# Optimization experiments

Measured on AMD Instinct MI355X. Metric: run time of the kernel, lower is better.

Reference implementation:

```python
import jax, jax.numpy as jnp
import numpy as np

B, S, D = 2, 1024, 1024
H, HD = 16, 64          # n_heads, head_dim (H*HD == D)
E, FF = 8, 2816         # num_experts, moe hidden_dim
TOP_K = 2               # hard-coded torch.topk(scores, 2)
EPS = 1e-5


def rmsnorm(x, w):
    return x * jax.lax.rsqrt(jnp.mean(x * x, axis=-1, keepdims=True) + EPS) * w


def apply_rope(x, cos, sin):
    # x: [B,S,H,HD]; cos/sin: [S,HD//2] -> interleaved rotary (llama style)
    xr, xi = x[..., 0::2], x[..., 1::2]
    c = cos[None, :, None, :]
    s = sin[None, :, None, :]
    out_r = xr * c - xi * s
    out_i = xr * s + xi * c
    return jnp.stack([out_r, out_i], axis=-1).reshape(x.shape)


def setup_inputs() -> dict:
    key = jax.random.key(0)
    ks = jax.random.split(key, 10)
    sc = 0.02
    pos = jnp.arange(S, dtype=jnp.float32)
    inv = 1.0 / (10000.0 ** (jnp.arange(0, HD, 2, dtype=jnp.float32) / HD))
    ang = pos[:, None] * inv[None, :]                       # [S, HD//2]
    return {
        "x": jax.random.normal(ks[0], (B, S, D), jnp.float32),
        "freqs_cos": jnp.cos(ang),
        "freqs_sin": jnp.sin(ang),
        "attn_norm_w": jnp.ones((D,), jnp.float32),
        "wq": jax.random.normal(ks[1], (D, D), jnp.float32) * sc,
        "wk": jax.random.normal(ks[2], (D, D), jnp.float32) * sc,
        "wv": jax.random.normal(ks[3], (D, D), jnp.float32) * sc,
        "wo": jax.random.normal(ks[4], (D, D), jnp.float32) * sc,
        "ffn_norm_w": jnp.ones((D,), jnp.float32),
        "gate_w": jax.random.normal(ks[5], (E, D), jnp.float32) * sc,
        "w1": jax.random.normal(ks[6], (E, FF, D), jnp.float32) * sc,
        "w2": jax.random.normal(ks[7], (E, FF, D), jnp.float32) * sc,
        "w3": jax.random.normal(ks[8], (E, FF, D), jnp.float32) * sc,
    }


def reference(x, freqs_cos, freqs_sin, attn_norm_w, wq, wk, wv, wo,
              ffn_norm_w, gate_w, w1, w2, w3):
    b, s, d = x.shape

    # ---- pre-norm attention + residual ----
    xn = rmsnorm(x, attn_norm_w)
    q = (xn @ wq.T).reshape(b, s, H, HD)
    k = (xn @ wk.T).reshape(b, s, H, HD)
    v = (xn @ wv.T).reshape(b, s, H, HD)
    q = apply_rope(q, freqs_cos, freqs_sin)
    k = apply_rope(k, freqs_cos, freqs_sin)
    scores = jnp.einsum("bqhd,bkhd->bhqk", q, k) / jnp.sqrt(jnp.float32(HD))
    causal = jnp.tril(jnp.ones((s, s), bool))
    scores = jnp.where(causal[None, None], scores, jnp.finfo(scores.dtype).min)
    attn = jax.nn.softmax(scores, axis=-1)
    o = jnp.einsum("bhqk,bkhd->bqhd", attn, v).reshape(b, s, d) @ wo.T
    h = x + o

    # ---- top-2 MoE FFN (math identical to gather-per-token einsums) ----
    t = rmsnorm(h, ffn_norm_w).reshape(-1, d)               # [T, D]
    T = t.shape[0]
    gate = t @ gate_w.T                                     # [T, E]
    expert_weights, expert_idx = jax.lax.top_k(gate, TOP_K)
    expert_weights = jax.nn.softmax(expert_weights, axis=-1)  # [T, 2]

    x1 = jax.nn.silu(jnp.einsum("td,efd->tef", t, w1))      # [T, E, FF]
    x3 = jnp.einsum("td,efd->tef", t, w3)                   # [T, E, FF]
    ta = jnp.arange(T)[:, None]
    g = x1[ta, expert_idx] * x3[ta, expert_idx]             # [T, 2, FF]
    gw = g * expert_weights[..., None]                      # fold routing weights
    h_full = jnp.zeros((T, E, FF), t.dtype).at[ta, expert_idx].add(gw)
    moe = jnp.einsum("tef,efd->td", h_full, w2)             # [T, D]

    return h + moe.reshape(b, s, d)
```

## Files before the change

### kernel.cpp

```cpp
#include <hip/hip_runtime.h>

#define DI __device__ __forceinline__

typedef __attribute__((ext_vector_type(8))) short short8;
typedef __attribute__((ext_vector_type(4))) float f32x4;

#define DM   1024
#define TT   2048
#define SEQ  1024
#define NHD  16
#define HDD  64
#define NE   8
#define FF   2816

DI ushort f2bf(float f){
  union { float f; unsigned u; } c; c.f = f;
  unsigned u = c.u;
  u += 0x7fffu + ((u >> 16) & 1u);
  return (ushort)(u >> 16);
}
DI float bf2f(ushort b){
  union { unsigned u; float f; } c; c.u = ((unsigned)b) << 16;
  return c.f;
}
DI unsigned pk2(float a, float b){ return (unsigned)f2bf(a) | ((unsigned)f2bf(b) << 16); }
DI uint2 mku2(unsigned a, unsigned b){ uint2 r; r.x = a; r.y = b; return r; }

DI f32x4 MFMA(short8 a, short8 b, f32x4 c){
  return __builtin_amdgcn_mfma_f32_16x16x32_bf16(a, b, c, 0, 0, 0);
}

DI void gload16(const void* g, void* l){
  __builtin_amdgcn_global_load_lds(
      (const __attribute__((address_space(1))) unsigned*)g,
      (__attribute__((address_space(3))) unsigned*)l, 16, 0, 0);
}

#define LDSWZB(row, p) (((row) * 128) + ((((p) ^ ((row) & 7))) * 16))

__global__ __launch_bounds__(256) void k_rmsnorm(const float* __restrict__ x,
                                                 const float* __restrict__ w,
                                                 ushort* __restrict__ xh,
                                                 ushort* __restrict__ xl)
{
  int row = blockIdx.x, tid = threadIdx.x;
  float4 v = ((const float4*)(x + (size_t)row * DM))[tid];
  float ss = v.x*v.x + v.y*v.y + v.z*v.z + v.w*v.w;
#pragma unroll
  for (int m = 32; m >= 1; m >>= 1) ss += __shfl_xor(ss, m);
  __shared__ float sh[4];
  if ((tid & 63) == 0) sh[tid >> 6] = ss;
  __syncthreads();
  ss = sh[0] + sh[1] + sh[2] + sh[3];
  float rstd = 1.0f / sqrtf(ss * (1.0f / DM) + 1e-5f);
  float4 wv = ((const float4*)w)[tid];
  float o0 = v.x * rstd * wv.x, o1 = v.y * rstd * wv.y;
  float o2 = v.z * rstd * wv.z, o3 = v.w * rstd * wv.w;
  ushort h0 = f2bf(o0), h1 = f2bf(o1), h2 = f2bf(o2), h3 = f2bf(o3);
  ((uint2*)(xh + (size_t)row * DM))[tid] =
      mku2((unsigned)h0 | ((unsigned)h1 << 16), (unsigned)h2 | ((unsigned)h3 << 16));
  ((uint2*)(xl + (size_t)row * DM))[tid] =
      mku2(pk2(o0 - bf2f(h0), o1 - bf2f(h1)), pk2(o2 - bf2f(h2), o3 - bf2f(h3)));
}

__global__ __launch_bounds__(256) void k_wsplit(
    const float* __restrict__ wq, const float* __restrict__ wk,
    const float* __restrict__ wv, const float* __restrict__ wo,
    ushort* __restrict__ qh, ushort* __restrict__ ql,
    ushort* __restrict__ kh, ushort* __restrict__ kl,
    ushort* __restrict__ vh, ushort* __restrict__ vl,
    ushort* __restrict__ oh, ushort* __restrict__ ol)
{
  int y = blockIdx.y;
  const float* W = y == 0 ? wq : (y == 1 ? wk : (y == 2 ? wv : wo));
  ushort* H = y == 0 ? qh : (y == 1 ? kh : (y == 2 ? vh : oh));
  ushort* L = y == 0 ? ql : (y == 1 ? kl : (y == 2 ? vl : ol));
  int i = blockIdx.x * 256 + threadIdx.x;
  float4 v = ((const float4*)W)[i];
  ushort h0 = f2bf(v.x), h1 = f2bf(v.y), h2 = f2bf(v.z), h3 = f2bf(v.w);
  ((uint2*)H)[i] = mku2((unsigned)h0 | ((unsigned)h1 << 16),
                        (unsigned)h2 | ((unsigned)h3 << 16));
  ((uint2*)L)[i] = mku2(pk2(v.x - bf2f(h0), v.y - bf2f(h1)),
                        pk2(v.z - bf2f(h2), v.w - bf2f(h3)));
}

__global__ __launch_bounds__(256, 2) void k_gemm_qkv(
    const ushort* __restrict__ xh, const ushort* __restrict__ xl,
    const ushort* __restrict__ wqh, const ushort* __restrict__ wql,
    const ushort* __restrict__ wkh, const ushort* __restrict__ wkl,
    const ushort* __restrict__ wvh, const ushort* __restrict__ wvl,
    float* __restrict__ qf, float* __restrict__ kf,
    ushort* __restrict__ vh, ushort* __restrict__ vl)
{
  __shared__ __align__(16) char lds[65536];
  char* Ah = lds;          char* Al = lds + 16384;
  char* Bh = lds + 32768;  char* Bl = lds + 49152;
  int bn = blockIdx.x, bm = blockIdx.y;
  int which = bn >> 3, bnn = bn & 7;
  const ushort* WH = which == 0 ? wqh : (which == 1 ? wkh : wvh);
  const ushort* WL = which == 0 ? wql : (which == 1 ? wkl : wvl);
  int tid = threadIdx.x, lane = tid & 63, w = tid >> 6, wr = w >> 1, wc = w & 1;
  int r0 = lane >> 3, pp = lane & 7;
  size_t asrc[4], bsrc[4]; int cdst[4];
#pragma unroll
  for (int i = 0; i < 4; i++) {
    int c = w * 4 + i;
    int row = c * 8 + r0;
    asrc[i] = (size_t)(bm * 128 + row) * DM + (pp ^ r0) * 8;
    bsrc[i] = (size_t)(bnn * 128 + row) * DM + (pp ^ r0) * 8;
    cdst[i] = c * 1024;
  }
  f32x4 acc[4][4] = {};
  for (int kb = 0; kb < DM; kb += 64) {
    __syncthreads();
#pragma unroll
    for (int i = 0; i < 4; i++) {
      gload16(xh + asrc[i] + kb, Ah + cdst[i]);
      gload16(xl + asrc[i] + kb, Al + cdst[i]);
      gload16(WH + bsrc[i] + kb, Bh + cdst[i]);
      gload16(WL + bsrc[i] + kb, Bl + cdst[i]);
    }
    __syncthreads();
#pragma unroll
    for (int kk = 0; kk < 2; kk++) {
      int j = kk * 4 + (lane >> 4);
      short8 ar[4], al[4];
#pragma unroll
      for (int mi = 0; mi < 4; mi++) {
        int row = wr * 64 + mi * 16 + (lane & 15);
        ar[mi] = *(const short8*)(Ah + LDSWZB(row, j));
        al[mi] = *(const short8*)(Al + LDSWZB(row, j));
      }
#pragma unroll
      for (int ni = 0; ni < 4; ni++) {
        int n = wc * 64 + ni * 16 + (lane & 15);
        short8 b_h = *(const short8*)(Bh + LDSWZB(n, j));
        short8 b_l = *(const short8*)(Bl + LDSWZB(n, j));
#pragma unroll
        for (int mi = 0; mi < 4; mi++) {
          acc[mi][ni] = MFMA(ar[mi], b_h, acc[mi][ni]);
          acc[mi][ni] = MFMA(al[mi], b_h, acc[mi][ni]);
          acc[mi][ni] = MFMA(ar[mi], b_l, acc[mi][ni]);
        }
      }
    }
  }
#pragma unroll
  for (int mi = 0; mi < 4; mi++)
#pragma unroll
    for (int ni = 0; ni < 4; ni++)
#pragma unroll
      for (int r = 0; r < 4; r++) {
        int rg = bm*128 + wr*64 + mi*16 + (lane >> 4)*4 + r;
        int cg = bnn*128 + wc*64 + ni*16 + (lane & 15);
        float v = acc[mi][ni][r];
        if (which == 0)      qf[(size_t)rg * DM + cg] = v;
        else if (which == 1) kf[(size_t)rg * DM + cg] = v;
        else {
          int b = rg >> 10, s = rg & 1023, hh = cg >> 6, hd = cg & 63;
          size_t o = ((size_t)((b*NHD + hh)*HDD + hd)) * SEQ + s;
          ushort hv = f2bf(v);
          vh[o] = hv; vl[o] = f2bf(v - bf2f(hv));
        }
      }
}

__global__ __launch_bounds__(256) void k_rope(
    const float* __restrict__ qf, const float* __restrict__ kf,
    const float* __restrict__ fc, const float* __restrict__ fs,
    ushort* __restrict__ qh, ushort* __restrict__ ql,
    ushort* __restrict__ kh, ushort* __restrict__ kl)
{
  int t = blockIdx.x, tid = threadIdx.x;
  int b = t >> 10, s = t & 1023;
#pragma unroll
  for (int i = 0; i < 2; i++) {
    int p = tid + i*256;
    int hh = p >> 5, pi = p & 31;
    float c = fc[s*32 + pi], sn = fs[s*32 + pi];
    size_t o = ((size_t)(b*NHD + hh) * SEQ + s) * HDD + pi*2;
    {
      float2 v = *(const float2*)(qf + (size_t)t * DM + hh*HDD + pi*2);
      float r0 = v.x*c - v.y*sn, r1 = v.x*sn + v.y*c;
      ushort a0 = f2bf(r0), a1 = f2bf(r1);
      *(unsigned*)(qh + o) = (unsigned)a0 | ((unsigned)a1 << 16);
      *(unsigned*)(ql + o) = pk2(r0 - bf2f(a0), r1 - bf2f(a1));
    }
    {
      float2 v = *(const float2*)(kf + (size_t)t * DM + hh*HDD + pi*2);
      float r0 = v.x*c - v.y*sn, r1 = v.x*sn + v.y*c;
      ushort a0 = f2bf(r0), a1 = f2bf(r1);
      *(unsigned*)(kh + o) = (unsigned)a0 | ((unsigned)a1 << 16);
      *(unsigned*)(kl + o) = pk2(r0 - bf2f(a0), r1 - bf2f(a1));
    }
  }
}

__global__ __launch_bounds__(256) void k_attn(
    const ushort* __restrict__ qh_, const ushort* __restrict__ ql_,
    const ushort* __restrict__ kh_, const ushort* __restrict__ kl_,
    const ushort* __restrict__ vh_, const ushort* __restrict__ vl_,
    ushort* __restrict__ oh_, ushort* __restrict__ ol_)
{
  __shared__ __align__(16) ushort Kh[64*64], Kl[64*64], Vh[64*64], Vl[64*64];
  __shared__ __align__(16) ushort Ph[4*16*64], Pl[4*16*64];
  int qt = blockIdx.x, bh = blockIdx.y;
  int tid = threadIdx.x, lane = tid & 63, w = tid >> 6;
  short8 qfh[2], qfl[2];
  int qrow = qt*64 + w*16 + (lane & 15);
#pragma unroll
  for (int ks = 0; ks < 2; ks++) {
    size_t g = ((size_t)bh * SEQ + qrow) * HDD + ks*32 + (lane >> 4)*8;
    qfh[ks] = *(const short8*)(qh_ + g);
    qfl[ks] = *(const short8*)(ql_ + g);
  }
  f32x4 oacc[4] = {};
  float mrun[4], lrun[4];
#pragma unroll
  for (int r = 0; r < 4; r++) { mrun[r] = -1e30f; lrun[r] = 0.0f; }

  for (int kt = 0; kt <= qt; kt++) {
    __syncthreads();
#pragma unroll
    for (int i = 0; i < 2; i++) {
      int c = tid + i*256, row = c >> 3, sl = c & 7;
      int d = row*64 + ((sl + row) & 7) * 8;
      size_t gk = ((size_t)bh * SEQ + kt*64 + row) * HDD + sl*8;
      *(uint4*)&Kh[d] = *(const uint4*)(kh_ + gk);
      *(uint4*)&Kl[d] = *(const uint4*)(kl_ + gk);
      size_t gv = ((size_t)bh * HDD + row) * SEQ + kt*64 + sl*8;
      *(uint4*)&Vh[d] = *(const uint4*)(vh_ + gv);
      *(uint4*)&Vl[d] = *(const uint4*)(vl_ + gv);
    }
    __syncthreads();
    f32x4 sa[4] = {};
#pragma unroll
    for (int j = 0; j < 4; j++) {
#pragma unroll
      for (int ks = 0; ks < 2; ks++) {
        int kr = j*16 + (lane & 15);
        int d = kr*64 + (((ks*4 + (lane >> 4)) + kr) & 7) * 8;
        short8 b_h = *(const short8*)&Kh[d];
        short8 b_l = *(const short8*)&Kl[d];
        sa[j] = MFMA(qfh[ks], b_h, sa[j]);
        sa[j] = MFMA(qfl[ks], b_h, sa[j]);
        sa[j] = MFMA(qfh[ks], b_l, sa[j]);
      }
    }
    float sv[4][4];
#pragma unroll
    for (int j = 0; j < 4; j++)
#pragma unroll
      for (int r = 0; r < 4; r++) {
        float xx = sa[j][r] * 0.125f;
        if (kt == qt) {
          int kv = j*16 + (lane & 15), qi = w*16 + (lane >> 4)*4 + r;
          if (kv > qi) xx = -1e30f;
        }
        sv[j][r] = xx;
      }
#pragma unroll
    for (int r = 0; r < 4; r++) {
      float mx = fmaxf(fmaxf(sv[0][r], sv[1][r]), fmaxf(sv[2][r], sv[3][r]));
#pragma unroll
      for (int m = 8; m >= 1; m >>= 1) mx = fmaxf(mx, __shfl_xor(mx, m));
      float mn = fmaxf(mrun[r], mx);
      float alp = __expf(mrun[r] - mn);
      mrun[r] = mn;
      float rs = 0.0f;
#pragma unroll
      for (int j = 0; j < 4; j++) { float pv = __expf(sv[j][r] - mn); sv[j][r] = pv; rs += pv; }
#pragma unroll
      for (int m = 8; m >= 1; m >>= 1) rs += __shfl_xor(rs, m);
      lrun[r] = lrun[r] * alp + rs;
#pragma unroll
      for (int hf = 0; hf < 4; hf++) oacc[hf][r] *= alp;
    }
#pragma unroll
    for (int j = 0; j < 4; j++)
#pragma unroll
      for (int r = 0; r < 4; r++) {
        int row = (lane >> 4)*4 + r, col = j*16 + (lane & 15);
        int d = w*1024 + row*64 + (((col >> 3) ^ (row & 7)) * 8) + (col & 7);
        ushort hv = f2bf(sv[j][r]);
        Ph[d] = hv; Pl[d] = f2bf(sv[j][r] - bf2f(hv));
      }
#pragma unroll
    for (int hf = 0; hf < 4; hf++) {
#pragma unroll
      for (int ks = 0; ks < 2; ks++) {
        int prow = lane & 15;
        int pg = ((ks*4 + (lane >> 4)) ^ (prow & 7)) * 8;
        short8 pfh = *(const short8*)&Ph[w*1024 + prow*64 + pg];
        short8 pfl = *(const short8*)&Pl[w*1024 + prow*64 + pg];
        int vrow = hf*16 + (lane & 15);
        int vd = vrow*64 + (((ks*4 + (lane >> 4)) + vrow) & 7) * 8;
        short8 vfh = *(const short8*)&Vh[vd];
        short8 vfl = *(const short8*)&Vl[vd];
        oacc[hf] = MFMA(pfh, vfh, oacc[hf]);
        oacc[hf] = MFMA(pfl, vfh, oacc[hf]);
        oacc[hf] = MFMA(pfh, vfl, oacc[hf]);
      }
    }
  }
  int b = bh >> 4, h = bh & 15;
#pragma unroll
  for (int r = 0; r < 4; r++) {
    float li = 1.0f / lrun[r];
    int srow = qt*64 + w*16 + (lane >> 4)*4 + r;
#pragma unroll
    for (int hf = 0; hf < 4; hf++) {
      float v = oacc[hf][r] * li;
      size_t o = ((size_t)(b*SEQ + srow)) * DM + h*HDD + hf*16 + (lane & 15);
      ushort hv = f2bf(v);
      oh_[o] = hv; ol_[o] = f2bf(v - bf2f(hv));
    }
  }
}

__global__ __launch_bounds__(256, 2) void k_gemm_wo(
    const ushort* __restrict__ oh, const ushort* __restrict__ ol,
    const ushort* __restrict__ woh, const ushort* __restrict__ wol,
    const float* __restrict__ x, float* __restrict__ hb)
{
  __shared__ __align__(16) char lds[49152];
  char* Ah = lds;          char* Al = lds + 8192;
  char* Bh = lds + 16384;  char* Bl = lds + 32768;
  int bnn = blockIdx.x, bm = blockIdx.y;
  int tid = threadIdx.x, lane = tid & 63, w = tid >> 6;
  int r0 = lane >> 3, pp = lane & 7;
  size_t asrc[2]; int adst[2];
#pragma unroll
  for (int i = 0; i < 2; i++) {
    int c = w * 2 + i;
    int row = c * 8 + r0;
    asrc[i] = (size_t)(bm * 64 + row) * DM + (pp ^ r0) * 8;
    adst[i] = c * 1024;
  }
  size_t bsrc[4]; int bdst[4];
#pragma unroll
  for (int i = 0; i < 4; i++) {
    int c = w * 4 + i;
    int row = c * 8 + r0;
    bsrc[i] = (size_t)(bnn * 128 + row) * DM + (pp ^ r0) * 8;
    bdst[i] = c * 1024;
  }
  f32x4 acc[4][2] = {};
  for (int kb = 0; kb < DM; kb += 64) {
    __syncthreads();
#pragma unroll
    for (int i = 0; i < 2; i++) {
      gload16(oh + asrc[i] + kb, Ah + adst[i]);
      gload16(ol + asrc[i] + kb, Al + adst[i]);
    }
#pragma unroll
    for (int i = 0; i < 4; i++) {
      gload16(woh + bsrc[i] + kb, Bh + bdst[i]);
      gload16(wol + bsrc[i] + kb, Bl + bdst[i]);
    }
    __syncthreads();
#pragma unroll
    for (int kk = 0; kk < 2; kk++) {
      int j = kk * 4 + (lane >> 4);
      short8 ar[4], al[4];
#pragma unroll
      for (int mi = 0; mi < 4; mi++) {
        int row = mi * 16 + (lane & 15);
        ar[mi] = *(const short8*)(Ah + LDSWZB(row, j));
        al[mi] = *(const short8*)(Al + LDSWZB(row, j));
      }
#pragma unroll
      for (int ni = 0; ni < 2; ni++) {
        int n = w * 32 + ni * 16 + (lane & 15);
        short8 b_h = *(const short8*)(Bh + LDSWZB(n, j));
        short8 b_l = *(const short8*)(Bl + LDSWZB(n, j));
#pragma unroll
        for (int mi = 0; mi < 4; mi++) {
          acc[mi][ni] = MFMA(ar[mi], b_h, acc[mi][ni]);
          acc[mi][ni] = MFMA(al[mi], b_h, acc[mi][ni]);
          acc[mi][ni] = MFMA(ar[mi], b_l, acc[mi][ni]);
        }
      }
    }
  }
#pragma unroll
  for (int mi = 0; mi < 4; mi++)
#pragma unroll
    for (int ni = 0; ni < 2; ni++)
#pragma unroll
      for (int r = 0; r < 4; r++) {
        int rg = bm*64 + mi*16 + (lane >> 4)*4 + r;
        int cg = bnn*128 + w*32 + ni*16 + (lane & 15);
        hb[(size_t)rg * DM + cg] = x[(size_t)rg * DM + cg] + acc[mi][ni][r];
      }
}

__global__ __launch_bounds__(256) void k_gate(
    const float* __restrict__ hb, const float* __restrict__ fw, const float* __restrict__ gwt,
    ushort* __restrict__ tb, int* __restrict__ idx, float* __restrict__ ew, int* __restrict__ cnt)
{
  int t = blockIdx.x, tid = threadIdx.x;
  float4 v = ((const float4*)(hb + (size_t)t * DM))[tid];
  float ss = v.x*v.x + v.y*v.y + v.z*v.z + v.w*v.w;
#pragma unroll
  for (int m = 32; m >= 1; m >>= 1) ss += __shfl_xor(ss, m);
  __shared__ float sh[4];
  if ((tid & 63) == 0) sh[tid >> 6] = ss;
  __syncthreads();
  ss = sh[0] + sh[1] + sh[2] + sh[3];
  float rstd = 1.0f / sqrtf(ss * (1.0f / DM) + 1e-5f);
  float4 wv = ((const float4*)fw)[tid];
  float tv0 = v.x*rstd*wv.x, tv1 = v.y*rstd*wv.y, tv2 = v.z*rstd*wv.z, tv3 = v.w*rstd*wv.w;
  ((uint2*)(tb + (size_t)t * DM))[tid] = mku2(pk2(tv0, tv1), pk2(tv2, tv3));
  float ge[8];
#pragma unroll
  for (int e = 0; e < 8; e++) {
    float4 gv = ((const float4*)(gwt + (size_t)e * DM))[tid];
    float s = tv0*gv.x + tv1*gv.y + tv2*gv.z + tv3*gv.w;
#pragma unroll
    for (int m = 32; m >= 1; m >>= 1) s += __shfl_xor(s, m);
    ge[e] = s;
  }
  __shared__ float gsh[4][8];
  if ((tid & 63) == 0) {
#pragma unroll
    for (int e = 0; e < 8; e++) gsh[tid >> 6][e] = ge[e];
  }
  __syncthreads();
  if (tid == 0) {
    float lg[8];
#pragma unroll
    for (int e = 0; e < 8; e++) lg[e] = gsh[0][e] + gsh[1][e] + gsh[2][e] + gsh[3][e];
    int i0 = 0;
    for (int e = 1; e < 8; e++) if (lg[e] > lg[i0]) i0 = e;
    int i1 = (i0 == 0) ? 1 : 0;
    for (int e = 0; e < 8; e++) if (e != i0 && lg[e] > lg[i1]) i1 = e;
    float ex = __expf(lg[i1] - lg[i0]);
    idx[2*t] = i0; idx[2*t+1] = i1;
    ew[2*t] = 1.0f / (1.0f + ex); ew[2*t+1] = ex / (1.0f + ex);
    atomicAdd(&cnt[i0], 1); atomicAdd(&cnt[i1], 1);
  }
}

__global__ void k_offsets(const int* __restrict__ cnt, int* __restrict__ off,
                          int* __restrict__ fil, int* __restrict__ tmap)
{
  if (threadIdx.x == 0 && blockIdx.x == 0) {
    int a = 0, nt = 0;
    for (int e = 0; e < 8; e++) {
      off[e] = a; a += cnt[e]; fil[e] = 0;
      int m = (cnt[e] + 255) >> 8;
      for (int j = 0; j < m; j++) { tmap[1 + nt] = (e << 8) | j; nt++; }
    }
    tmap[0] = nt;
  }
}

__global__ __launch_bounds__(256) void k_scatter(
    const int* __restrict__ idx, const int* __restrict__ off,
    int* __restrict__ fil, int* __restrict__ ent, int* __restrict__ pos)
{
  int t = blockIdx.x * 256 + threadIdx.x;
  if (t < TT) {
#pragma unroll
    for (int k = 0; k < 2; k++) {
      int e = idx[2*t + k];
      int p = atomicAdd(&fil[e], 1);
      int g = off[e] + p;
      ent[g] = 2*t + k;
      pos[2*t + k] = g;
    }
  }
}

__global__ __launch_bounds__(256) void k_tw2(const float* __restrict__ w2, ushort* __restrict__ w2t)
{
  int dt = blockIdx.x, ft = blockIdx.y, e = blockIdx.z;
  __shared__ ushort lt[64*72];
  int tid = threadIdx.x;
#pragma unroll
  for (int i = 0; i < 4; i++) {
    int c = tid + i*256;
    int r = c >> 4, q = c & 15;
    float4 v = *(const float4*)(w2 + ((size_t)e*FF + ft*64 + r) * DM + dt*64 + q*4);
    lt[(q*4+0)*72 + r] = f2bf(v.x);
    lt[(q*4+1)*72 + r] = f2bf(v.y);
    lt[(q*4+2)*72 + r] = f2bf(v.z);
    lt[(q*4+3)*72 + r] = f2bf(v.w);
  }
  __syncthreads();
#pragma unroll
  for (int i = 0; i < 2; i++) {
    int c = tid + i*256;
    int d = c >> 3, fq = c & 7;
    *(uint4*)(w2t + ((size_t)e*DM + dt*64 + d) * FF + ft*64 + fq*8) = *(const uint4*)&lt[d*72 + fq*8];
  }
}

__global__ __launch_bounds__(512, 4) void k_moe13(
    const ushort* __restrict__ tb, const float* __restrict__ w1, const float* __restrict__ w3,
    const int* __restrict__ ent, const float* __restrict__ ew,
    const int* __restrict__ cnt, const int* __restrict__ off, const int* __restrict__ tmap,
    ushort* __restrict__ gb)
{
  int y = blockIdx.y;
  if (y >= tmap[0]) return;
  int tm = tmap[1 + y];
  int e = tm >> 8, mt = tm & 255;
  int nt = blockIdx.x;
  int cn = cnt[e], oe = off[e];
  __shared__ __align__(16) char lds[49152];
  char* Ab  = lds;
  char* B1b = lds + 32768;
  char* B3b = lds + 40960;
  int tid = threadIdx.x, lane = tid & 63, w = tid >> 6;
  int wr = w >> 1, wc = w & 1;
  const ushort* abase = tb + (((lane & 7) ^ (lane >> 3)) * 8);
  unsigned aoff[4];
#pragma unroll
  for (int i = 0; i < 4; i++) {
    int c = w * 4 + i;
    int r = c * 8 + (lane >> 3);
    int g = oe + mt * 256 + r; if (g > 2*TT - 1) g = 2*TT - 1;
    aoff[i] = (unsigned)((ent[g] >> 1) * DM);
  }
  int brow = tid >> 3, bp = tid & 7;
  const float* b1src = w1 + ((size_t)e * FF + nt * 64 + brow) * DM + bp * 8;
  const float* b3src = w3 + ((size_t)e * FF + nt * 64 + brow) * DM + bp * 8;
  int bdst = LDSWZB(brow, bp);
  f32x4 acc1[4][2] = {}, acc3[4][2] = {};
  for (int kb = 0; kb < DM; kb += 64) {
    __syncthreads();
#pragma unroll
    for (int i = 0; i < 4; i++)
      gload16(abase + aoff[i] + kb, Ab + (w * 4 + i) * 1024);
    {
      float4 va = *(const float4*)(b1src + kb);
      float4 vb = *(const float4*)(b1src + kb + 4);
      float4 vc = *(const float4*)(b3src + kb);
      float4 vd = *(const float4*)(b3src + kb + 4);
      uint4 p1, p3;
      p1.x = pk2(va.x, va.y); p1.y = pk2(va.z, va.w);
      p1.z = pk2(vb.x, vb.y); p1.w = pk2(vb.z, vb.w);
      p3.x = pk2(vc.x, vc.y); p3.y = pk2(vc.z, vc.w);
      p3.z = pk2(vd.x, vd.y); p3.w = pk2(vd.z, vd.w);
      *(uint4*)(B1b + bdst) = p1;
      *(uint4*)(B3b + bdst) = p3;
    }
    __syncthreads();
#pragma unroll
    for (int kk = 0; kk < 2; kk++) {
      int j = kk * 4 + (lane >> 4);
      short8 af[4];
#pragma unroll
      for (int mi = 0; mi < 4; mi++) {
        int row = wr * 64 + mi * 16 + (lane & 15);
        af[mi] = *(const short8*)(Ab + LDSWZB(row, j));
      }
#pragma unroll
      for (int ni = 0; ni < 2; ni++) {
        int n = wc * 32 + ni * 16 + (lane & 15);
        short8 b1f = *(const short8*)(B1b + LDSWZB(n, j));
        short8 b3f = *(const short8*)(B3b + LDSWZB(n, j));
#pragma unroll
        for (int mi = 0; mi < 4; mi++) {
          acc1[mi][ni] = MFMA(af[mi], b1f, acc1[mi][ni]);
          acc3[mi][ni] = MFMA(af[mi], b3f, acc3[mi][ni]);
        }
      }
    }
  }
#pragma unroll
  for (int mi = 0; mi < 4; mi++)
#pragma unroll
    for (int ni = 0; ni < 2; ni++)
#pragma unroll
      for (int r = 0; r < 4; r++) {
        int grow = mt * 256 + wr * 64 + mi * 16 + (lane >> 4) * 4 + r;
        if (grow < cn) {
          int g = oe + grow;
          float gwv = ew[ent[g]];
          int f = nt * 64 + wc * 32 + ni * 16 + (lane & 15);
          float x1 = acc1[mi][ni][r], x3 = acc3[mi][ni][r];
          float sg = x1 / (1.0f + __expf(-x1));
          gb[(size_t)g * FF + f] = f2bf(sg * x3 * gwv);
        }
      }
}

__global__ __launch_bounds__(512, 4) void k_moe2(
    const ushort* __restrict__ gb, const ushort* __restrict__ w2t,
    const int* __restrict__ cnt, const int* __restrict__ off, const int* __restrict__ tmap,
    float* __restrict__ mr)
{
  int y = blockIdx.y;
  if (y >= tmap[0]) return;
  int tm = tmap[1 + y];
  int e = tm >> 8, mt = tm & 255;
  int nt = blockIdx.x;
  int cn = cnt[e], oe = off[e];
  __shared__ __align__(16) char lds[40960];
  char* Ab = lds; char* Bb = lds + 32768;
  int tid = threadIdx.x, lane = tid & 63, w = tid >> 6;

  const ushort* abase = gb + (((lane & 7) ^ (lane >> 3)) * 8);
  unsigned aoff[4];
#pragma unroll
  for (int i = 0; i < 4; i++) {
    int c = w * 4 + i;
    int r = c * 8 + (lane >> 3);
    int g = oe + mt * 256 + r; if (g > 2*TT - 1) g = 2*TT - 1;
    aoff[i] = (unsigned)(g * FF);
  }
  const ushort* bsrc = w2t + ((size_t)e * DM + nt * 64 + (w * 8 + (lane >> 3))) * FF
                       + (((lane & 7) ^ (lane >> 3)) * 8);
  void* bdst = Bb + w * 1024;

  f32x4 acc[2][4] = {};
  for (int kb = 0; kb < FF; kb += 64) {
    __syncthreads();
#pragma unroll
    for (int i = 0; i < 4; i++)
      gload16(abase + aoff[i] + kb, Ab + (w * 4 + i) * 1024);
    gload16(bsrc + kb, bdst);
    __syncthreads();
#pragma unroll
    for (int kk = 0; kk < 2; kk++) {
      short8 af[2], bf[4];
#pragma unroll
      for (int mi = 0; mi < 2; mi++) {
        int row = w * 32 + mi * 16 + (lane & 15);
        af[mi] = *(const short8*)(Ab + LDSWZB(row, kk * 4 + (lane >> 4)));
      }
#pragma unroll
      for (int ni = 0; ni < 4; ni++) {
        int n = ni * 16 + (lane & 15);
        bf[ni] = *(const short8*)(Bb + LDSWZB(n, kk * 4 + (lane >> 4)));
      }
#pragma unroll
      for (int ni = 0; ni < 4; ni++)
#pragma unroll
        for (int mi = 0; mi < 2; mi++)
          acc[mi][ni] = MFMA(af[mi], bf[ni], acc[mi][ni]);
    }
  }
#pragma unroll
  for (int mi = 0; mi < 2; mi++)
#pragma unroll
    for (int ni = 0; ni < 4; ni++)
#pragma unroll
      for (int r = 0; r < 4; r++) {
        int grow = mt * 256 + w * 32 + mi * 16 + (lane >> 4) * 4 + r;
        if (grow < cn) {
          int cg = nt * 64 + ni * 16 + (lane & 15);
          mr[(size_t)(oe + grow) * DM + cg] = acc[mi][ni][r];
        }
      }
}

__global__ __launch_bounds__(256) void k_final(
    const float* __restrict__ hb, const float* __restrict__ mr,
    const int* __restrict__ pos, float* __restrict__ out)
{
  int t = blockIdx.x, tid = threadIdx.x;
  int g0 = pos[2*t], g1 = pos[2*t+1];
  float4 a  = ((const float4*)(hb + (size_t)t * DM))[tid];
  float4 m0 = ((const float4*)(mr + (size_t)g0 * DM))[tid];
  float4 m1 = ((const float4*)(mr + (size_t)g1 * DM))[tid];
  float4 o;
  o.x = a.x + m0.x + m1.x; o.y = a.y + m0.y + m1.y;
  o.z = a.z + m0.z + m1.z; o.w = a.w + m0.w + m1.w;
  ((float4*)(out + (size_t)t * DM))[tid] = o;
}

extern "C" void kernel_launch(void* const* d_in, const int* in_sizes, int n_in,
                              void* d_out, int out_size, void* d_ws, size_t ws_size,
                              hipStream_t stream)
{
  const float* x   = (const float*)d_in[0];
  const float* fc  = (const float*)d_in[1];
  const float* fs  = (const float*)d_in[2];
  const float* anw = (const float*)d_in[3];
  const float* wq  = (const float*)d_in[4];
  const float* wk  = (const float*)d_in[5];
  const float* wv  = (const float*)d_in[6];
  const float* wo  = (const float*)d_in[7];
  const float* fnw = (const float*)d_in[8];
  const float* gwm = (const float*)d_in[9];
  const float* w1  = (const float*)d_in[10];
  const float* w2  = (const float*)d_in[11];
  const float* w3  = (const float*)d_in[12];
  float* out = (float*)d_out;

  char* p = (char*)d_ws;
  auto alloc = [&](size_t n) { char* r = p; p += (n + 255) & ~(size_t)255; return r; };
  ushort* xnh = (ushort*)alloc((size_t)TT*DM*2);
  ushort* xnl = (ushort*)alloc((size_t)TT*DM*2);
  float*  qf  = (float*) alloc((size_t)TT*DM*4);
  float*  kf  = (float*) alloc((size_t)TT*DM*4);
  ushort* qh  = (ushort*)alloc((size_t)TT*DM*2);
  ushort* ql  = (ushort*)alloc((size_t)TT*DM*2);
  ushort* kh  = (ushort*)alloc((size_t)TT*DM*2);
  ushort* kl  = (ushort*)alloc((size_t)TT*DM*2);
  ushort* vh  = (ushort*)alloc((size_t)TT*DM*2);
  ushort* vl  = (ushort*)alloc((size_t)TT*DM*2);
  ushort* oh  = (ushort*)alloc((size_t)TT*DM*2);
  ushort* ol  = (ushort*)alloc((size_t)TT*DM*2);
  float*  hb  = (float*) alloc((size_t)TT*DM*4);
  ushort* tb  = (ushort*)alloc((size_t)TT*DM*2);
  ushort* w2t = (ushort*)alloc((size_t)NE*FF*DM*2);
  ushort* gb  = (ushort*)alloc((size_t)2*TT*FF*2);
  float*  mr  = (float*) alloc((size_t)2*TT*DM*4);
  int*    idx = (int*)   alloc((size_t)2*TT*4);
  float*  ew  = (float*) alloc((size_t)2*TT*4);
  int*    ent = (int*)   alloc((size_t)2*TT*4);
  int*    pos = (int*)   alloc((size_t)2*TT*4);
  int*    cnt = (int*)   alloc(32);
  int*    off = (int*)   alloc(32);
  int*    fil = (int*)   alloc(32);
  int*    tmap= (int*)   alloc(256);

  ushort* wsp = (ushort*)mr;
  const size_t WN = (size_t)DM * DM;
  ushort* wqh = wsp;        ushort* wql = wsp + WN;
  ushort* wkh = wsp + 2*WN; ushort* wkl = wsp + 3*WN;
  ushort* wvh = wsp + 4*WN; ushort* wvl = wsp + 5*WN;
  ushort* woh = wsp + 6*WN; ushort* wol = wsp + 7*WN;

  hipMemsetAsync(cnt, 0, 32, stream);
  k_rmsnorm<<<TT, 256, 0, stream>>>(x, anw, xnh, xnl);
  k_wsplit<<<dim3(1024, 4), 256, 0, stream>>>(wq, wk, wv, wo,
      wqh, wql, wkh, wkl, wvh, wvl, woh, wol);
  k_tw2<<<dim3(16, 44, 8), 256, 0, stream>>>(w2, w2t);
  k_gemm_qkv<<<dim3(24, 16), 256, 0, stream>>>(xnh, xnl,
      wqh, wql, wkh, wkl, wvh, wvl, qf, kf, vh, vl);
  k_rope<<<TT, 256, 0, stream>>>(qf, kf, fc, fs, qh, ql, kh, kl);
  k_attn<<<dim3(16, 32), 256, 0, stream>>>(qh, ql, kh, kl, vh, vl, oh, ol);
  k_gemm_wo<<<dim3(8, 32), 256, 0, stream>>>(oh, ol, woh, wol, x, hb);
  k_gate<<<TT, 256, 0, stream>>>(hb, fnw, gwm, tb, idx, ew, cnt);
  k_offsets<<<1, 64, 0, stream>>>(cnt, off, fil, tmap);
  k_scatter<<<8, 256, 0, stream>>>(idx, off, fil, ent, pos);
  k_moe13<<<dim3(44, 24), 512, 0, stream>>>(tb, w1, w3, ent, ew, cnt, off, tmap, gb);
  k_moe2<<<dim3(16, 24), 512, 0, stream>>>(gb, w2t, cnt, off, tmap, mr);
  k_final<<<TT, 256, 0, stream>>>(hb, mr, pos, out);
  (void)in_sizes; (void)n_in; (void)out_size; (void)ws_size;
}
```

Before: 460.1 us.

## Double-buffer LDS tiles in MoE GEMM kernels to overlap loads with MFMA

Converts the k_moe13 and k_moe2 K-loops to a double-buffered scheme with one barrier per iteration. The next tile's global-to-LDS loads (and register prefetch of fp32 w1/w3 rows) are issued before computing on the current buffer, so memory latency can hide behind MFMA work. LDS usage doubles (96KB and 80KB), which cuts blocks per CU, and launch bounds are relaxed to match. The last iteration wraps around and issues a redundant prefetch of tile 0. Correctness depends on the async gload16 completing before the next iteration's single barrier.

Measured after the change: 481.4 us. +4.6%, slower.

```diff
diff --git a/kernel.cpp b/kernel.cpp
--- a/kernel.cpp
+++ b/kernel.cpp
@@ -497,7 +497,7 @@
   }
 }
 
-__global__ __launch_bounds__(512, 4) void k_moe13(
+__global__ __launch_bounds__(512) void k_moe13(
     const ushort* __restrict__ tb, const float* __restrict__ w1, const float* __restrict__ w3,
     const int* __restrict__ ent, const float* __restrict__ ew,
     const int* __restrict__ cnt, const int* __restrict__ off, const int* __restrict__ tmap,
@@ -509,10 +509,7 @@
   int e = tm >> 8, mt = tm & 255;
   int nt = blockIdx.x;
   int cn = cnt[e], oe = off[e];
-  __shared__ __align__(16) char lds[49152];
-  char* Ab  = lds;
-  char* B1b = lds + 32768;
-  char* B3b = lds + 40960;
+  __shared__ __align__(16) char lds[98304];
   int tid = threadIdx.x, lane = tid & 63, w = tid >> 6;
   int wr = w >> 1, wc = w & 1;
   const ushort* abase = tb + (((lane & 7) ^ (lane >> 3)) * 8);
@@ -528,26 +525,40 @@
   const float* b1src = w1 + ((size_t)e * FF + nt * 64 + brow) * DM + bp * 8;
   const float* b3src = w3 + ((size_t)e * FF + nt * 64 + brow) * DM + bp * 8;
   int bdst = LDSWZB(brow, bp);
+
+#pragma unroll
+  for (int i = 0; i < 4; i++)
+    gload16(abase + aoff[i], lds + (w * 4 + i) * 1024);
+  float4 rb1x = *(const float4*)(b1src);
+  float4 rb1y = *(const float4*)(b1src + 4);
+  float4 rb3x = *(const float4*)(b3src);
+  float4 rb3y = *(const float4*)(b3src + 4);
+
   f32x4 acc1[4][2] = {}, acc3[4][2] = {};
-  for (int kb = 0; kb < DM; kb += 64) {
+#pragma unroll 2
+  for (int t = 0; t < 16; t++) {
+    int cur = t & 1;
+    char* Ab  = lds + cur * 32768;
+    char* B1b = lds + 65536 + cur * 8192;
+    char* B3b = lds + 81920 + cur * 8192;
+    uint4 p1, p3;
+    p1.x = pk2(rb1x.x, rb1x.y); p1.y = pk2(rb1x.z, rb1x.w);
+    p1.z = pk2(rb1y.x, rb1y.y); p1.w = pk2(rb1y.z, rb1y.w);
+    p3.x = pk2(rb3x.x, rb3x.y); p3.y = pk2(rb3x.z, rb3x.w);
+    p3.z = pk2(rb3y.x, rb3y.y); p3.w = pk2(rb3y.z, rb3y.w);
+    *(uint4*)(B1b + bdst) = p1;
+    *(uint4*)(B3b + bdst) = p3;
     __syncthreads();
+    int t2 = (t + 1) & 15;
+    int kb2 = t2 * 64;
+    char* An = lds + (t2 & 1) * 32768;
 #pragma unroll
     for (int i = 0; i < 4; i++)
-      gload16(abase + aoff[i] + kb, Ab + (w * 4 + i) * 1024);
-    {
-      float4 va = *(const float4*)(b1src + kb);
-      float4 vb = *(const float4*)(b1src + kb + 4);
-      float4 vc = *(const float4*)(b3src + kb);
-      float4 vd = *(const float4*)(b3src + kb + 4);
-      uint4 p1, p3;
-      p1.x = pk2(va.x, va.y); p1.y = pk2(va.z, va.w);
-      p1.z = pk2(vb.x, vb.y); p1.w = pk2(vb.z, vb.w);
-      p3.x = pk2(vc.x, vc.y); p3.y = pk2(vc.z, vc.w);
-      p3.z = pk2(vd.x, vd.y); p3.w = pk2(vd.z, vd.w);
-      *(uint4*)(B1b + bdst) = p1;
-      *(uint4*)(B3b + bdst) = p3;
-    }
-    __syncthreads();
+      gload16(abase + aoff[i] + kb2, An + (w * 4 + i) * 1024);
+    rb1x = *(const float4*)(b1src + kb2);
+    rb1y = *(const float4*)(b1src + kb2 + 4);
+    rb3x = *(const float4*)(b3src + kb2);
+    rb3y = *(const float4*)(b3src + kb2 + 4);
 #pragma unroll
     for (int kk = 0; kk < 2; kk++) {
       int j = kk * 4 + (lane >> 4);
@@ -588,7 +599,7 @@
       }
 }
 
-__global__ __launch_bounds__(512, 4) void k_moe2(
+__global__ __launch_bounds__(512, 2) void k_moe2(
     const ushort* __restrict__ gb, const ushort* __restrict__ w2t,
     const int* __restrict__ cnt, const int* __restrict__ off, const int* __restrict__ tmap,
     float* __restrict__ mr)
@@ -599,8 +610,7 @@
   int e = tm >> 8, mt = tm & 255;
   int nt = blockIdx.x;
   int cn = cnt[e], oe = off[e];
-  __shared__ __align__(16) char lds[40960];
-  char* Ab = lds; char* Bb = lds + 32768;
+  __shared__ __align__(16) char lds[81920];
   int tid = threadIdx.x, lane = tid & 63, w = tid >> 6;
 
   const ushort* abase = gb + (((lane & 7) ^ (lane >> 3)) * 8);
@@ -614,16 +624,27 @@
   }
   const ushort* bsrc = w2t + ((size_t)e * DM + nt * 64 + (w * 8 + (lane >> 3))) * FF
                        + (((lane & 7) ^ (lane >> 3)) * 8);
-  void* bdst = Bb + w * 1024;
+
+#pragma unroll
+  for (int i = 0; i < 4; i++)
+    gload16(abase + aoff[i], lds + (w * 4 + i) * 1024);
+  gload16(bsrc, lds + 65536 + w * 1024);
 
   f32x4 acc[2][4] = {};
-  for (int kb = 0; kb < FF; kb += 64) {
+#pragma unroll 2
+  for (int t = 0; t < 44; t++) {
+    int cur = t & 1;
+    char* Ab = lds + cur * 32768;
+    char* Bb = lds + 65536 + cur * 8192;
     __syncthreads();
+    int t2 = (t + 1 == 44) ? 0 : t + 1;
+    int kb2 = t2 * 64;
+    char* An = lds + (t2 & 1) * 32768;
+    char* Bn = lds + 65536 + (t2 & 1) * 8192;
 #pragma unroll
     for (int i = 0; i < 4; i++)
-      gload16(abase + aoff[i] + kb, Ab + (w * 4 + i) * 1024);
-    gload16(bsrc + kb, bdst);
-    __syncthreads();
+      gload16(abase + aoff[i] + kb2, An + (w * 4 + i) * 1024);
+    gload16(bsrc + kb2, Bn + w * 1024);
 #pragma unroll
     for (int kk = 0; kk < 2; kk++) {
       short8 af[2], bf[4];
```

## Double-buffer MoE GEMM tiles with async global-to-LDS loads

Applied to the files above, without the earlier changes.

Both MoE GEMM kernels now use two LDS buffers for the A and B tiles. The next-but-one stage is issued with global_load_lds while the current stage is computed, using explicit vmcnt waits and barriers in place of two __syncthreads per iteration. In k_moe13 the fp32 w1/w3 weights now go straight into LDS and are converted to bf16 after the LDS read, with the K step halved to 32. The goal is to hide global memory latency behind MFMA work. In exchange, LDS use per block grows to 64KB and 80KB, which cuts how many blocks fit on each CU.

Result: slower. 479.4 us (+4.2%).

```diff
diff --git a/kernel.cpp b/kernel.cpp
--- a/kernel.cpp
+++ b/kernel.cpp
@@ -37,6 +37,11 @@
 }
 
 #define LDSWZB(row, p) (((row) * 128) + ((((p) ^ ((row) & 7))) * 16))
+#define SW4(row, p)    (((row) * 64) + ((((p) ^ ((row) & 3))) * 16))
+
+#define VMCNT(N) asm volatile("s_waitcnt vmcnt(" #N ")" ::: "memory")
+#define SBAR()   __builtin_amdgcn_s_barrier()
+#define SCHED0() __builtin_amdgcn_sched_barrier(0)
 
 __global__ __launch_bounds__(256) void k_rmsnorm(const float* __restrict__ x,
                                                  const float* __restrict__ w,
@@ -509,67 +514,82 @@
   int e = tm >> 8, mt = tm & 255;
   int nt = blockIdx.x;
   int cn = cnt[e], oe = off[e];
-  __shared__ __align__(16) char lds[49152];
-  char* Ab  = lds;
-  char* B1b = lds + 32768;
-  char* B3b = lds + 40960;
+  __shared__ __align__(16) char lds[65536];
   int tid = threadIdx.x, lane = tid & 63, w = tid >> 6;
   int wr = w >> 1, wc = w & 1;
-  const ushort* abase = tb + (((lane & 7) ^ (lane >> 3)) * 8);
-  unsigned aoff[4];
-#pragma unroll
-  for (int i = 0; i < 4; i++) {
-    int c = w * 4 + i;
-    int r = c * 8 + (lane >> 3);
+
+  const ushort* abase = tb + (((lane & 3) ^ ((lane >> 2) & 3)) * 8);
+  unsigned aoff[2];
+#pragma unroll
+  for (int i = 0; i < 2; i++) {
+    int c = 2 * w + i;
+    int r = c * 16 + (lane >> 2);
     int g = oe + mt * 256 + r; if (g > 2*TT - 1) g = 2*TT - 1;
     aoff[i] = (unsigned)((ent[g] >> 1) * DM);
   }
-  int brow = tid >> 3, bp = tid & 7;
-  const float* b1src = w1 + ((size_t)e * FF + nt * 64 + brow) * DM + bp * 8;
-  const float* b3src = w3 + ((size_t)e * FF + nt * 64 + brow) * DM + bp * 8;
-  int bdst = LDSWZB(brow, bp);
+  size_t bofs = ((size_t)e * FF + nt * 64 + w * 8 + (lane >> 3)) * DM
+              + (((lane & 7) ^ (lane >> 3)) * 4);
+  const float* b1p = w1 + bofs;
+  const float* b3p = w3 + bofs;
+
   f32x4 acc1[4][2] = {}, acc3[4][2] = {};
-  for (int kb = 0; kb < DM; kb += 64) {
-    __syncthreads();
-#pragma unroll
-    for (int i = 0; i < 4; i++)
-      gload16(abase + aoff[i] + kb, Ab + (w * 4 + i) * 1024);
-    {
-      float4 va = *(const float4*)(b1src + kb);
-      float4 vb = *(const float4*)(b1src + kb + 4);
-      float4 vc = *(const float4*)(b3src + kb);
-      float4 vd = *(const float4*)(b3src + kb + 4);
+
+  auto stage = [&](int t) {
+    int kb = t * 32;
+    char* Ab = lds + (t & 1) * 16384;
+    char* B1 = lds + 32768 + (t & 1) * 8192;
+    char* B3 = lds + 49152 + (t & 1) * 8192;
+    gload16(abase + aoff[0] + kb, Ab + (2 * w) * 1024);
+    gload16(abase + aoff[1] + kb, Ab + (2 * w + 1) * 1024);
+    gload16(b1p + kb, B1 + w * 1024);
+    gload16(b3p + kb, B3 + w * 1024);
+  };
+
+  stage(0); stage(1);
+  VMCNT(4); SBAR(); SCHED0();
+
+#pragma unroll 2
+  for (int t = 0; t < 32; t++) {
+    char* Ab = lds + (t & 1) * 16384;
+    char* B1 = lds + 32768 + (t & 1) * 8192;
+    char* B3 = lds + 49152 + (t & 1) * 8192;
+    int j = lane >> 4;
+    short8 af[4];
+#pragma unroll
+    for (int mi = 0; mi < 4; mi++) {
+      int row = wr * 64 + mi * 16 + (lane & 15);
+      af[mi] = *(const short8*)(Ab + SW4(row, j));
+    }
+#pragma unroll
+    for (int ni = 0; ni < 2; ni++) {
+      int n = wc * 32 + ni * 16 + (lane & 15);
+      f32x4 u0 = *(const f32x4*)(B1 + LDSWZB(n, 2 * j));
+      f32x4 u1 = *(const f32x4*)(B1 + LDSWZB(n, 2 * j + 1));
+      f32x4 v0 = *(const f32x4*)(B3 + LDSWZB(n, 2 * j));
+      f32x4 v1 = *(const f32x4*)(B3 + LDSWZB(n, 2 * j + 1));
       uint4 p1, p3;
-      p1.x = pk2(va.x, va.y); p1.y = pk2(va.z, va.w);
-      p1.z = pk2(vb.x, vb.y); p1.w = pk2(vb.z, vb.w);
-      p3.x = pk2(vc.x, vc.y); p3.y = pk2(vc.z, vc.w);
-      p3.z = pk2(vd.x, vd.y); p3.w = pk2(vd.z, vd.w);
-      *(uint4*)(B1b + bdst) = p1;
-      *(uint4*)(B3b + bdst) = p3;
-    }
-    __syncthreads();
-#pragma unroll
-    for (int kk = 0; kk < 2; kk++) {
-      int j = kk * 4 + (lane >> 4);
-      short8 af[4];
+      p1.x = pk2(u0[0], u0[1]); p1.y = pk2(u0[2], u0[3]);
+      p1.z = pk2(u1[0], u1[1]); p1.w = pk2(u1[2], u1[3]);
+      p3.x = pk2(v0[0], v0[1]); p3.y = pk2(v0[2], v0[3]);
+      p3.z = pk2(v1[0], v1[1]); p3.w = pk2(v1[2], v1[3]);
+      short8 b1f, b3f;
+      *(uint4*)&b1f = p1; *(uint4*)&b3f = p3;
 #pragma unroll
       for (int mi = 0; mi < 4; mi++) {
-        int row = wr * 64 + mi * 16 + (lane & 15);
-        af[mi] = *(const short8*)(Ab + LDSWZB(row, j));
-      }
-#pragma unroll
-      for (int ni = 0; ni < 2; ni++) {
-        int n = wc * 32 + ni * 16 + (lane & 15);
-        short8 b1f = *(const short8*)(B1b + LDSWZB(n, j));
-        short8 b3f = *(const short8*)(B3b + LDSWZB(n, j));
-#pragma unroll
-        for (int mi = 0; mi < 4; mi++) {
-          acc1[mi][ni] = MFMA(af[mi], b1f, acc1[mi][ni]);
-          acc3[mi][ni] = MFMA(af[mi], b3f, acc3[mi][ni]);
-        }
-      }
-    }
-  }
+        acc1[mi][ni] = MFMA(af[mi], b1f, acc1[mi][ni]);
+        acc3[mi][ni] = MFMA(af[mi], b3f, acc3[mi][ni]);
+      }
+    }
+    SBAR(); SCHED0();
+    if (t + 2 < 32) {
+      stage(t + 2);
+      VMCNT(4);
+    } else {
+      VMCNT(0);
+    }
+    SBAR(); SCHED0();
+  }
+
 #pragma unroll
   for (int mi = 0; mi < 4; mi++)
 #pragma unroll
@@ -599,8 +619,7 @@
   int e = tm >> 8, mt = tm & 255;
   int nt = blockIdx.x;
   int cn = cnt[e], oe = off[e];
-  __shared__ __align__(16) char lds[40960];
-  char* Ab = lds; char* Bb = lds + 32768;
+  __shared__ __align__(16) char lds[81920];
   int tid = threadIdx.x, lane = tid & 63, w = tid >> 6;
 
   const ushort* abase = gb + (((lane & 7) ^ (lane >> 3)) * 8);
@@ -614,16 +633,25 @@
   }
   const ushort* bsrc = w2t + ((size_t)e * DM + nt * 64 + (w * 8 + (lane >> 3))) * FF
                        + (((lane & 7) ^ (lane >> 3)) * 8);
-  void* bdst = Bb + w * 1024;
-
-  f32x4 acc[2][4] = {};
-  for (int kb = 0; kb < FF; kb += 64) {
-    __syncthreads();
+
+  auto stage = [&](int t) {
+    int kb = t * 64;
+    char* Ab = lds + (t & 1) * 32768;
+    char* Bb = lds + 65536 + (t & 1) * 8192;
 #pragma unroll
     for (int i = 0; i < 4; i++)
       gload16(abase + aoff[i] + kb, Ab + (w * 4 + i) * 1024);
-    gload16(bsrc + kb, bdst);
-    __syncthreads();
+    gload16(bsrc + kb, Bb + w * 1024);
+  };
+
+  stage(0); stage(1);
+  VMCNT(5); SBAR(); SCHED0();
+
+  f32x4 acc[2][4] = {};
+#pragma unroll 2
+  for (int t = 0; t < 44; t++) {
+    char* Ab = lds + (t & 1) * 32768;
+    char* Bb = lds + 65536 + (t & 1) * 8192;
 #pragma unroll
     for (int kk = 0; kk < 2; kk++) {
       short8 af[2], bf[4];
@@ -643,7 +671,16 @@
         for (int mi = 0; mi < 2; mi++)
           acc[mi][ni] = MFMA(af[mi], bf[ni], acc[mi][ni]);
     }
-  }
+    SBAR(); SCHED0();
+    if (t + 2 < 44) {
+      stage(t + 2);
+      VMCNT(5);
+    } else {
+      VMCNT(0);
+    }
+    SBAR(); SCHED0();
+  }
+
 #pragma unroll
   for (int mi = 0; mi < 2; mi++)
 #pragma unroll
```

## Pre-convert w1/w3 to bf16 and halve MoE row tiles to 128

Applied to the files above, without the earlier changes.

Adds a kernel that converts the fp32 w1 and w3 expert weights to bf16 once per call. This lets k_moe13 stage them with direct 16-byte async loads instead of loading fp32 and converting in registers inside every tile. Both MoE GEMMs shrink from 512 to 256 threads and from 256-row to 128-row tiles, which doubles the tile count and grid size so more blocks can run when experts hold few tokens. The cost is an extra pass over about 46M weights per call plus a bf16 buffer placed at the start of the workspace, and each weight tile is now re-read by twice as many row tiles.

Measured after the change: 458.5 us. Within noise of the previous version (-0.4%).

```diff
diff --git a/kernel.cpp b/kernel.cpp
--- a/kernel.cpp
+++ b/kernel.cpp
@@ -84,6 +84,21 @@
                         pk2(v.z - bf2f(h2), v.w - bf2f(h3)));
 }
 
+__global__ __launch_bounds__(256) void k_cw13(const float* __restrict__ w1,
+                                              const float* __restrict__ w3,
+                                              ushort* __restrict__ w1b,
+                                              ushort* __restrict__ w3b)
+{
+  const float* src = blockIdx.y ? w3 : w1;
+  ushort* dst = blockIdx.y ? w3b : w1b;
+  const size_t N4 = (size_t)NE * FF * DM / 4;
+  for (size_t i = (size_t)blockIdx.x * 256 + threadIdx.x; i < N4;
+       i += (size_t)gridDim.x * 256) {
+    float4 v = ((const float4*)src)[i];
+    ((uint2*)dst)[i] = mku2(pk2(v.x, v.y), pk2(v.z, v.w));
+  }
+}
+
 __global__ __launch_bounds__(256, 2) void k_gemm_qkv(
     const ushort* __restrict__ xh, const ushort* __restrict__ xl,
     const ushort* __restrict__ wqh, const ushort* __restrict__ wql,
@@ -449,7 +464,7 @@
     int a = 0, nt = 0;
     for (int e = 0; e < 8; e++) {
       off[e] = a; a += cnt[e]; fil[e] = 0;
-      int m = (cnt[e] + 255) >> 8;
+      int m = (cnt[e] + 127) >> 7;
       for (int j = 0; j < m; j++) { tmap[1 + nt] = (e << 8) | j; nt++; }
     }
     tmap[0] = nt;
@@ -497,8 +512,8 @@
   }
 }
 
-__global__ __launch_bounds__(512, 4) void k_moe13(
-    const ushort* __restrict__ tb, const float* __restrict__ w1, const float* __restrict__ w3,
+__global__ __launch_bounds__(256, 4) void k_moe13(
+    const ushort* __restrict__ tb, const ushort* __restrict__ w1b, const ushort* __restrict__ w3b,
     const int* __restrict__ ent, const float* __restrict__ ew,
     const int* __restrict__ cnt, const int* __restrict__ off, const int* __restrict__ tmap,
     ushort* __restrict__ gb)
@@ -509,43 +524,41 @@
   int e = tm >> 8, mt = tm & 255;
   int nt = blockIdx.x;
   int cn = cnt[e], oe = off[e];
-  __shared__ __align__(16) char lds[49152];
-  char* Ab  = lds;
-  char* B1b = lds + 32768;
-  char* B3b = lds + 40960;
+  __shared__ __align__(16) char lds[32768];
+  char* Ab = lds;
+  char* B1 = lds + 16384;
+  char* B3 = lds + 24576;
   int tid = threadIdx.x, lane = tid & 63, w = tid >> 6;
   int wr = w >> 1, wc = w & 1;
-  const ushort* abase = tb + (((lane & 7) ^ (lane >> 3)) * 8);
+  int r0 = lane >> 3, pp = lane & 7;
+
+  const ushort* abase = tb + (pp ^ r0) * 8;
   unsigned aoff[4];
 #pragma unroll
   for (int i = 0; i < 4; i++) {
     int c = w * 4 + i;
-    int r = c * 8 + (lane >> 3);
-    int g = oe + mt * 256 + r; if (g > 2*TT - 1) g = 2*TT - 1;
+    int r = c * 8 + r0;
+    int g = oe + mt * 128 + r; if (g > 2*TT - 1) g = 2*TT - 1;
     aoff[i] = (unsigned)((ent[g] >> 1) * DM);
   }
-  int brow = tid >> 3, bp = tid & 7;
-  const float* b1src = w1 + ((size_t)e * FF + nt * 64 + brow) * DM + bp * 8;
-  const float* b3src = w3 + ((size_t)e * FF + nt * 64 + brow) * DM + bp * 8;
-  int bdst = LDSWZB(brow, bp);
+  size_t bofs[2];
+#pragma unroll
+  for (int i = 0; i < 2; i++) {
+    int c = 2 * w + i;
+    bofs[i] = ((size_t)e * FF + nt * 64 + c * 8 + r0) * DM + (pp ^ r0) * 8;
+  }
+
   f32x4 acc1[4][2] = {}, acc3[4][2] = {};
+
   for (int kb = 0; kb < DM; kb += 64) {
     __syncthreads();
 #pragma unroll
     for (int i = 0; i < 4; i++)
       gload16(abase + aoff[i] + kb, Ab + (w * 4 + i) * 1024);
-    {
-      float4 va = *(const float4*)(b1src + kb);
-      float4 vb = *(const float4*)(b1src + kb + 4);
-      float4 vc = *(const float4*)(b3src + kb);
-      float4 vd = *(const float4*)(b3src + kb + 4);
-      uint4 p1, p3;
-      p1.x = pk2(va.x, va.y); p1.y = pk2(va.z, va.w);
-      p1.z = pk2(vb.x, vb.y); p1.w = pk2(vb.z, vb.w);
-      p3.x = pk2(vc.x, vc.y); p3.y = pk2(vc.z, vc.w);
-      p3.z = pk2(vd.x, vd.y); p3.w = pk2(vd.z, vd.w);
-      *(uint4*)(B1b + bdst) = p1;
-      *(uint4*)(B3b + bdst) = p3;
+#pragma unroll
+    for (int i = 0; i < 2; i++) {
+      gload16(w1b + bofs[i] + kb, B1 + (2 * w + i) * 1024);
+      gload16(w3b + bofs[i] + kb, B3 + (2 * w + i) * 1024);
     }
     __syncthreads();
 #pragma unroll
@@ -560,8 +573,8 @@
 #pragma unroll
       for (int ni = 0; ni < 2; ni++) {
         int n = wc * 32 + ni * 16 + (lane & 15);
-        short8 b1f = *(const short8*)(B1b + LDSWZB(n, j));
-        short8 b3f = *(const short8*)(B3b + LDSWZB(n, j));
+        short8 b1f = *(const short8*)(B1 + LDSWZB(n, j));
+        short8 b3f = *(const short8*)(B3 + LDSWZB(n, j));
 #pragma unroll
         for (int mi = 0; mi < 4; mi++) {
           acc1[mi][ni] = MFMA(af[mi], b1f, acc1[mi][ni]);
@@ -576,7 +589,7 @@
     for (int ni = 0; ni < 2; ni++)
 #pragma unroll
       for (int r = 0; r < 4; r++) {
-        int grow = mt * 256 + wr * 64 + mi * 16 + (lane >> 4) * 4 + r;
+        int grow = mt * 128 + wr * 64 + mi * 16 + (lane >> 4) * 4 + r;
         if (grow < cn) {
           int g = oe + grow;
           float gwv = ew[ent[g]];
@@ -588,7 +601,7 @@
       }
 }
 
-__global__ __launch_bounds__(512, 4) void k_moe2(
+__global__ __launch_bounds__(256, 4) void k_moe2(
     const ushort* __restrict__ gb, const ushort* __restrict__ w2t,
     const int* __restrict__ cnt, const int* __restrict__ off, const int* __restrict__ tmap,
     float* __restrict__ mr)
@@ -599,49 +612,58 @@
   int e = tm >> 8, mt = tm & 255;
   int nt = blockIdx.x;
   int cn = cnt[e], oe = off[e];
-  __shared__ __align__(16) char lds[40960];
-  char* Ab = lds; char* Bb = lds + 32768;
+  __shared__ __align__(16) char lds[24576];
+  char* Ab = lds; char* Bb = lds + 16384;
   int tid = threadIdx.x, lane = tid & 63, w = tid >> 6;
-
-  const ushort* abase = gb + (((lane & 7) ^ (lane >> 3)) * 8);
+  int r0 = lane >> 3, pp = lane & 7;
+
+  const ushort* abase = gb + (pp ^ r0) * 8;
   unsigned aoff[4];
 #pragma unroll
   for (int i = 0; i < 4; i++) {
     int c = w * 4 + i;
-    int r = c * 8 + (lane >> 3);
-    int g = oe + mt * 256 + r; if (g > 2*TT - 1) g = 2*TT - 1;
+    int r = c * 8 + r0;
+    int g = oe + mt * 128 + r; if (g > 2*TT - 1) g = 2*TT - 1;
     aoff[i] = (unsigned)(g * FF);
   }
-  const ushort* bsrc = w2t + ((size_t)e * DM + nt * 64 + (w * 8 + (lane >> 3))) * FF
-                       + (((lane & 7) ^ (lane >> 3)) * 8);
-  void* bdst = Bb + w * 1024;
-
-  f32x4 acc[2][4] = {};
+  size_t bofs[2];
+#pragma unroll
+  for (int i = 0; i < 2; i++) {
+    int c = 2 * w + i;
+    bofs[i] = ((size_t)e * DM + nt * 64 + c * 8 + r0) * FF + (pp ^ r0) * 8;
+  }
+
+  f32x4 acc[4][1] = {};
+  f32x4 a2[2][4] = {};
+  (void)acc;
   for (int kb = 0; kb < FF; kb += 64) {
     __syncthreads();
 #pragma unroll
     for (int i = 0; i < 4; i++)
       gload16(abase + aoff[i] + kb, Ab + (w * 4 + i) * 1024);
-    gload16(bsrc + kb, bdst);
+#pragma unroll
+    for (int i = 0; i < 2; i++)
+      gload16(w2t + bofs[i] + kb, Bb + (2 * w + i) * 1024);
     __syncthreads();
 #pragma unroll
     for (int kk = 0; kk < 2; kk++) {
+      int j = kk * 4 + (lane >> 4);
       short8 af[2], bf[4];
 #pragma unroll
       for (int mi = 0; mi < 2; mi++) {
         int row = w * 32 + mi * 16 + (lane & 15);
-        af[mi] = *(const short8*)(Ab + LDSWZB(row, kk * 4 + (lane >> 4)));
+        af[mi] = *(const short8*)(Ab + LDSWZB(row, j));
       }
 #pragma unroll
       for (int ni = 0; ni < 4; ni++) {
         int n = ni * 16 + (lane & 15);
-        bf[ni] = *(const short8*)(Bb + LDSWZB(n, kk * 4 + (lane >> 4)));
+        bf[ni] = *(const short8*)(Bb + LDSWZB(n, j));
       }
 #pragma unroll
       for (int ni = 0; ni < 4; ni++)
 #pragma unroll
         for (int mi = 0; mi < 2; mi++)
-          acc[mi][ni] = MFMA(af[mi], bf[ni], acc[mi][ni]);
+          a2[mi][ni] = MFMA(af[mi], bf[ni], a2[mi][ni]);
     }
   }
 #pragma unroll
@@ -650,10 +672,10 @@
     for (int ni = 0; ni < 4; ni++)
 #pragma unroll
       for (int r = 0; r < 4; r++) {
-        int grow = mt * 256 + w * 32 + mi * 16 + (lane >> 4) * 4 + r;
+        int grow = mt * 128 + w * 32 + mi * 16 + (lane >> 4) * 4 + r;
         if (grow < cn) {
           int cg = nt * 64 + ni * 16 + (lane & 15);
-          mr[(size_t)(oe + grow) * DM + cg] = acc[mi][ni][r];
+          mr[(size_t)(oe + grow) * DM + cg] = a2[mi][ni][r];
         }
       }
 }
@@ -727,6 +749,9 @@
   ushort* wvh = wsp + 4*WN; ushort* wvl = wsp + 5*WN;
   ushort* woh = wsp + 6*WN; ushort* wol = wsp + 7*WN;
 
+  ushort* w1b = (ushort*)d_ws;
+  ushort* w3b = (ushort*)alloc((size_t)NE*FF*DM*2);
+
   hipMemsetAsync(cnt, 0, 32, stream);
   k_rmsnorm<<<TT, 256, 0, stream>>>(x, anw, xnh, xnl);
   k_wsplit<<<dim3(1024, 4), 256, 0, stream>>>(wq, wk, wv, wo,
@@ -740,8 +765,9 @@
   k_gate<<<TT, 256, 0, stream>>>(hb, fnw, gwm, tb, idx, ew, cnt);
   k_offsets<<<1, 64, 0, stream>>>(cnt, off, fil, tmap);
   k_scatter<<<8, 256, 0, stream>>>(idx, off, fil, ent, pos);
-  k_moe13<<<dim3(44, 24), 512, 0, stream>>>(tb, w1, w3, ent, ew, cnt, off, tmap, gb);
-  k_moe2<<<dim3(16, 24), 512, 0, stream>>>(gb, w2t, cnt, off, tmap, mr);
+  k_cw13<<<dim3(2048, 2), 256, 0, stream>>>(w1, w3, w1b, w3b);
+  k_moe13<<<dim3(44, 48), 256, 0, stream>>>(tb, w1b, w3b, ent, ew, cnt, off, tmap, gb);
+  k_moe2<<<dim3(16, 48), 256, 0, stream>>>(gb, w2t, cnt, off, tmap, mr);
   k_final<<<TT, 256, 0, stream>>>(hb, mr, pos, out);
   (void)in_sizes; (void)n_in; (void)out_size; (void)ws_size;
 }
```
